# Performance work log

Hardware: AMD Instinct MI355X
Metric: run time of the kernel (lower is better)

Reference implementation:

```python
import jax, jax.numpy as jnp
import numpy as np

N_USERS = 100000
N_ITEMS = 50000
DIM = 64
N_EDGES = 1000000
N_NODES = N_USERS + N_ITEMS


def setup_inputs() -> dict:
    key = jax.random.key(0)
    k1, k2, k3 = jax.random.split(key, 3)
    # nn.init.normal_(std=0.1)
    user_emb = jax.random.normal(k1, (N_USERS, DIM), dtype=jnp.float32) * 0.1
    item_emb = jax.random.normal(k2, (N_ITEMS, DIM), dtype=jnp.float32) * 0.1
    edge_index = jax.random.randint(k3, (2, N_EDGES), 0, N_NODES, dtype=jnp.int32)
    return {"user_emb": user_emb, "item_emb": item_emb,
            "edge_index": edge_index, "n_layers": 3}


def reference(user_emb, item_emb, edge_index, n_layers):
    """LightGCN.computer(): n_layers of LGConv with uniform-alpha residual sum."""
    num_users = user_emb.shape[0]
    x = jnp.concatenate([user_emb, item_emb], axis=0)  # [N, d]
    n = x.shape[0]
    src, dst = edge_index[0], edge_index[1]

    # gcn_norm without self-loops (PyG LGConv default): deg from dst (in-degree)
    deg = jax.ops.segment_sum(jnp.ones_like(dst, dtype=x.dtype), dst,
                              num_segments=n)  # [N]
    dinv = jnp.where(deg > 0, jax.lax.rsqrt(jnp.maximum(deg, 1.0)), 0.0)
    norm = dinv[src] * dinv[dst]  # [E]

    alpha = 1.0 / (n_layers + 1)
    out = x * alpha
    for _ in range(n_layers):
        msg = x[src] * norm[:, None]                          # gather + scale [E, d]
        x = jax.ops.segment_sum(msg, dst, num_segments=n)     # scatter-add  [N, d]
        out = out + x * alpha
    users = out[:num_users]
    items = out[num_users:]
    return users, items
```

## Files before the change

kernel.cpp:

```cpp
#include <hip/hip_runtime.h>


#define N_USERS_C 100000
#define NNODES_C  150000
#define DIM_C     64
#define NLAYERS_C 3

#define BSHIFT    10
#define BSIZE     1024
#define NB_BUCKET ((NNODES_C + BSIZE - 1) >> BSHIFT)
#define EPB       4096
#define NBLK_E    ((1000000 + EPB - 1) / EPB)
#define HIST_N    (NB_BUCKET * NBLK_E)
#define SCAN_L1B  ((HIST_N + 1023) / 1024)


__device__ __forceinline__ float bf2f(unsigned short u) {
    union { unsigned int i; float f; } c;
    c.i = ((unsigned int)u) << 16;
    return c.f;
}

__device__ __forceinline__ unsigned short f2bf(float f) {
    union { float f; unsigned int i; } c;
    c.f = f;
    unsigned int x = c.i;
    return (unsigned short)((x + 0x7fffu + ((x >> 16) & 1u)) >> 16);
}


__global__ void k_hist(const int* __restrict__ dst, int* __restrict__ hist, int nE) {
    __shared__ int sh[NB_BUCKET];
    for (int i = threadIdx.x; i < NB_BUCKET; i += 256) sh[i] = 0;
    __syncthreads();
    int gEnd = min((int)(blockIdx.x + 1) * (EPB / 4), nE / 4);
    for (int g = blockIdx.x * (EPB / 4) + threadIdx.x; g < gEnd; g += 256) {
        int4 d4 = *(const int4*)(dst + g * 4);
        atomicAdd(&sh[d4.x >> BSHIFT], 1);
        atomicAdd(&sh[d4.y >> BSHIFT], 1);
        atomicAdd(&sh[d4.z >> BSHIFT], 1);
        atomicAdd(&sh[d4.w >> BSHIFT], 1);
    }
    __syncthreads();
    for (int b = threadIdx.x; b < NB_BUCKET; b += 256)
        hist[b * NBLK_E + blockIdx.x] = sh[b];
}

__global__ void k_scan_l1(int* __restrict__ hist, int* __restrict__ l1sum) {
    __shared__ int sd[1024];
    int t = threadIdx.x;
    int i = blockIdx.x * 1024 + t;
    int v = (i < HIST_N) ? hist[i] : 0;
    sd[t] = v;
    __syncthreads();
    for (int o = 1; o < 1024; o <<= 1) {
        int u = (t >= o) ? sd[t - o] : 0;
        __syncthreads();
        sd[t] += u;
        __syncthreads();
    }
    if (i < HIST_N) hist[i] = sd[t] - v;
    if (t == 1023) l1sum[blockIdx.x] = sd[1023];
}

__global__ void k_scan_l2add(int* __restrict__ hist, const int* __restrict__ l1sum) {
    __shared__ int s_pre;
    int t = threadIdx.x;
    if (t < 64) {
        int v = (t < (int)blockIdx.x && t < SCAN_L1B) ? l1sum[t] : 0;
        #pragma unroll
        for (int m = 1; m < 64; m <<= 1) v += __shfl_xor(v, m);
        if (t == 0) s_pre = v;
    }
    __syncthreads();
    int i = blockIdx.x * 1024 + t;
    if (i < HIST_N) hist[i] += s_pre;
}

__global__ void k_bucket(const int* __restrict__ src, const int* __restrict__ dst,
                         const int* __restrict__ histS, unsigned int* __restrict__ staged,
                         int nE) {
    __shared__ int sc[NB_BUCKET];
    for (int b = threadIdx.x; b < NB_BUCKET; b += 256)
        sc[b] = histS[b * NBLK_E + blockIdx.x];
    __syncthreads();
    int gEnd = min((int)(blockIdx.x + 1) * (EPB / 4), nE / 4);
    for (int g = blockIdx.x * (EPB / 4) + threadIdx.x; g < gEnd; g += 256) {
        int4 s4 = *(const int4*)(src + g * 4);
        int4 d4 = *(const int4*)(dst + g * 4);
        int p;
        p = atomicAdd(&sc[d4.x >> BSHIFT], 1);
        staged[p] = ((unsigned int)s4.x << BSHIFT) | (unsigned int)(d4.x & (BSIZE - 1));
        p = atomicAdd(&sc[d4.y >> BSHIFT], 1);
        staged[p] = ((unsigned int)s4.y << BSHIFT) | (unsigned int)(d4.y & (BSIZE - 1));
        p = atomicAdd(&sc[d4.z >> BSHIFT], 1);
        staged[p] = ((unsigned int)s4.z << BSHIFT) | (unsigned int)(d4.z & (BSIZE - 1));
        p = atomicAdd(&sc[d4.w >> BSHIFT], 1);
        staged[p] = ((unsigned int)s4.w << BSHIFT) | (unsigned int)(d4.w & (BSIZE - 1));
    }
}

__global__ void k_csr(const int* __restrict__ histS, const unsigned int* __restrict__ staged,
                      int* __restrict__ off, int* __restrict__ csrS,
                      const float* __restrict__ ue, const float* __restrict__ ie,
                      unsigned short* __restrict__ T0,
                      int nE, int nNodes) {
    __shared__ int s_deg[BSIZE];
    __shared__ int s_off[BSIZE];
    __shared__ int s_p[256];
    int b = blockIdx.x;
    int t = threadIdx.x;
    int base = histS[b * NBLK_E];
    int end  = (b + 1 < NB_BUCKET) ? histS[(b + 1) * NBLK_E] : nE;
    int cnt  = end - base;

    for (int i = t; i < BSIZE; i += 256) s_deg[i] = 0;
    __syncthreads();
    for (int k = t; k < cnt; k += 256) {
        unsigned int w = staged[base + k];
        atomicAdd(&s_deg[w & (BSIZE - 1)], 1);
    }
    __syncthreads();
    int l0 = s_deg[t * 4], l1 = s_deg[t * 4 + 1], l2 = s_deg[t * 4 + 2], l3 = s_deg[t * 4 + 3];
    int psum = l0 + l1 + l2 + l3;
    s_p[t] = psum;
    __syncthreads();
    for (int o = 1; o < 256; o <<= 1) {
        int v = (t >= o) ? s_p[t - o] : 0;
        __syncthreads();
        s_p[t] += v;
        __syncthreads();
    }
    int ex = s_p[t] - psum;
    s_off[t * 4]     = ex;
    s_off[t * 4 + 1] = ex + l0;
    s_off[t * 4 + 2] = ex + l0 + l1;
    s_off[t * 4 + 3] = ex + l0 + l1 + l2;
    __syncthreads();
    int nodeBase = b << BSHIFT;
    for (int i = t; i < BSIZE; i += 256) {
        int node = nodeBase + i;
        if (node < nNodes) off[node] = base + s_off[i];
    }
    if (b == 0 && t == 0) off[nNodes] = nE;

    for (int g = t; g < BSIZE * 8; g += 256) {
        int nl   = g >> 3;
        int node = nodeBase + nl;
        if (node < nNodes) {
            int dg = s_deg[nl];
            float dv = (dg > 0) ? rsqrtf((float)dg) : 0.0f;
            int sub = g & 7;
            const float* eb = (node < N_USERS_C)
                ? (ue + (size_t)node * DIM_C + sub * 8)
                : (ie + (size_t)(node - N_USERS_C) * DIM_C + sub * 8);
            float4 A = *(const float4*)(eb);
            float4 B = *(const float4*)(eb + 4);
            uint4 o;
            o.x = (unsigned int)f2bf(A.x * dv) | ((unsigned int)f2bf(A.y * dv) << 16);
            o.y = (unsigned int)f2bf(A.z * dv) | ((unsigned int)f2bf(A.w * dv) << 16);
            o.z = (unsigned int)f2bf(B.x * dv) | ((unsigned int)f2bf(B.y * dv) << 16);
            o.w = (unsigned int)f2bf(B.z * dv) | ((unsigned int)f2bf(B.w * dv) << 16);
            *(uint4*)(T0 + (size_t)node * DIM_C + sub * 8) = o;
        }
    }
    __syncthreads();
    for (int i = t; i < BSIZE; i += 256) s_deg[i] = s_off[i];
    __syncthreads();
    for (int k = t; k < cnt; k += 256) {
        unsigned int w = staged[base + k];
        int slot = base + atomicAdd(&s_deg[w & (BSIZE - 1)], 1);
        csrS[slot] = (int)(w >> BSHIFT);
    }
}


__device__ __forceinline__ void add8(float* a, uint4 v) {
    a[0] += bf2f((unsigned short)(v.x & 0xffff));
    a[1] += bf2f((unsigned short)(v.x >> 16));
    a[2] += bf2f((unsigned short)(v.y & 0xffff));
    a[3] += bf2f((unsigned short)(v.y >> 16));
    a[4] += bf2f((unsigned short)(v.z & 0xffff));
    a[5] += bf2f((unsigned short)(v.z >> 16));
    a[6] += bf2f((unsigned short)(v.w & 0xffff));
    a[7] += bf2f((unsigned short)(v.w >> 16));
}

__device__ __forceinline__ void fma8(float* a, uint4 v, float w) {
    a[0] += w * bf2f((unsigned short)(v.x & 0xffff));
    a[1] += w * bf2f((unsigned short)(v.x >> 16));
    a[2] += w * bf2f((unsigned short)(v.y & 0xffff));
    a[3] += w * bf2f((unsigned short)(v.y >> 16));
    a[4] += w * bf2f((unsigned short)(v.z & 0xffff));
    a[5] += w * bf2f((unsigned short)(v.z >> 16));
    a[6] += w * bf2f((unsigned short)(v.w & 0xffff));
    a[7] += w * bf2f((unsigned short)(v.w >> 16));
}

template <int FINAL>
__global__ void k_gather(const int* __restrict__ off, const int* __restrict__ csrS,
                         const unsigned short* __restrict__ T,
                         unsigned short* __restrict__ Tn,
                         const float* __restrict__ ue, const float* __restrict__ ie,
                         const unsigned short* __restrict__ T1,
                         const unsigned short* __restrict__ T2,
                         float* __restrict__ outp, float alpha, int nNodes) {
    int t = blockIdx.x * blockDim.x + threadIdx.x;
    int w = t >> 6;
    int lane = t & 63;
    int half = lane >> 5;
    int sub  = lane & 31;
    int slot = sub >> 3;
    int q    = sub & 7;
    int node = w * 2 + half;
    if (node >= nNodes) return;

    int b = off[node];
    int e = off[node + 1];

    float a[8] = {0.f, 0.f, 0.f, 0.f, 0.f, 0.f, 0.f, 0.f};

    for (int jj = b; jj < e; jj += 4) {
        int j = jj + slot;
        if (j < e) {
            int s = csrS[j];
            uint4 v = *(const uint4*)(T + (size_t)s * DIM_C + q * 8);
            add8(a, v);
        }
    }

    #pragma unroll
    for (int m = 8; m <= 16; m <<= 1) {
        #pragma unroll
        for (int k = 0; k < 8; ++k) a[k] += __shfl_xor(a[k], m);
    }

    if (slot == 0) {
        size_t idx = (size_t)node * DIM_C + q * 8;
        float degf = (float)(e - b);
        if (FINAL) {
            float sd = sqrtf(degf);
            float dv = (e > b) ? rsqrtf(degf) : 0.0f;
            const float* ob = (node < N_USERS_C)
                ? (ue + (size_t)node * DIM_C + q * 8)
                : (ie + (size_t)(node - N_USERS_C) * DIM_C + q * 8);
            float4 x0a = *(const float4*)(ob);
            float4 x0b = *(const float4*)(ob + 4);
            uint4 u1 = *(const uint4*)(T1 + idx);
            uint4 u2 = *(const uint4*)(T2 + idx);
            float r[8] = {0.f, 0.f, 0.f, 0.f, 0.f, 0.f, 0.f, 0.f};
            fma8(r, u1, sd);
            fma8(r, u2, sd);
            float4 o0, o1;
            o0.x = alpha * (x0a.x + r[0] + dv * a[0]);
            o0.y = alpha * (x0a.y + r[1] + dv * a[1]);
            o0.z = alpha * (x0a.z + r[2] + dv * a[2]);
            o0.w = alpha * (x0a.w + r[3] + dv * a[3]);
            o1.x = alpha * (x0b.x + r[4] + dv * a[4]);
            o1.y = alpha * (x0b.y + r[5] + dv * a[5]);
            o1.z = alpha * (x0b.z + r[6] + dv * a[6]);
            o1.w = alpha * (x0b.w + r[7] + dv * a[7]);
            *(float4*)(outp + idx)     = o0;
            *(float4*)(outp + idx + 4) = o1;
        } else {
            float inv = (e > b) ? (1.0f / degf) : 0.0f;
            uint4 o;
            o.x = (unsigned int)f2bf(a[0] * inv) | ((unsigned int)f2bf(a[1] * inv) << 16);
            o.y = (unsigned int)f2bf(a[2] * inv) | ((unsigned int)f2bf(a[3] * inv) << 16);
            o.z = (unsigned int)f2bf(a[4] * inv) | ((unsigned int)f2bf(a[5] * inv) << 16);
            o.w = (unsigned int)f2bf(a[6] * inv) | ((unsigned int)f2bf(a[7] * inv) << 16);
            *(uint4*)(Tn + idx) = o;
        }
    }
}


__global__ void k_count_deg_fb(const int* __restrict__ dst, int* __restrict__ deg, int nE) {
    int e = blockIdx.x * blockDim.x + threadIdx.x;
    if (e < nE) atomicAdd(&deg[dst[e]], 1);
}

__global__ void k_dinv_fb(const int* __restrict__ deg, float* __restrict__ dinv, int n) {
    int i = blockIdx.x * blockDim.x + threadIdx.x;
    if (i < n) {
        int d = deg[i];
        dinv[i] = (d > 0) ? rsqrtf((float)d) : 0.0f;
    }
}

__global__ void k_init_fb(const float4* __restrict__ ue, const float4* __restrict__ ie,
                          float4* __restrict__ x, float4* __restrict__ out,
                          float alpha, int n4u, int n4) {
    int i = blockIdx.x * blockDim.x + threadIdx.x;
    if (i < n4) {
        float4 v = (i < n4u) ? ue[i] : ie[i - n4u];
        x[i] = v;
        out[i] = make_float4(v.x * alpha, v.y * alpha, v.z * alpha, v.w * alpha);
    }
}

__global__ void k_scatter(const int* __restrict__ src, const int* __restrict__ dst,
                          const float* __restrict__ dinv, const float* __restrict__ x,
                          float* __restrict__ y, int nE) {
    int t = blockIdx.x * blockDim.x + threadIdx.x;
    int e = t >> 4;
    int q = t & 15;
    if (e >= nE) return;
    int s = src[e];
    int d = dst[e];
    float w = dinv[s] * dinv[d];
    float4 v = *(const float4*)(x + (size_t)s * DIM_C + q * 4);
    float* yp = y + (size_t)d * DIM_C + q * 4;
    atomicAdd(yp + 0, v.x * w);
    atomicAdd(yp + 1, v.y * w);
    atomicAdd(yp + 2, v.z * w);
    atomicAdd(yp + 3, v.w * w);
}

__global__ void k_accum(const float4* __restrict__ y, float4* __restrict__ out,
                        float alpha, int n4) {
    int i = blockIdx.x * blockDim.x + threadIdx.x;
    if (i < n4) {
        float4 v = y[i];
        float4 o = out[i];
        o.x += v.x * alpha;
        o.y += v.y * alpha;
        o.z += v.z * alpha;
        o.w += v.w * alpha;
        out[i] = o;
    }
}


extern "C" void kernel_launch(void* const* d_in, const int* in_sizes, int n_in,
                              void* d_out, int out_size, void* d_ws, size_t ws_size,
                              hipStream_t stream) {
    const float* user_emb = (const float*)d_in[0];
    const float* item_emb = (const float*)d_in[1];
    const int*   edge     = (const int*)d_in[2];

    const int nE = in_sizes[2] / 2;
    const int* src = edge;
    const int* dst = edge + nE;

    const int nNodes = NNODES_C;
    const int nElems = nNodes * DIM_C;
    const int n4     = nElems / 4;
    const int n4u    = N_USERS_C * DIM_C / 4;
    const float alpha = 1.0f / (NLAYERS_C + 1);
    float* out = (float*)d_out;

    const size_t REQ = 66344448;

    char* ws = (char*)d_ws;

    if (ws_size >= REQ) {
        int*            hist   = (int*)           (ws);
        int*            l1sum  = (int*)           (ws + 144064);
        unsigned int*   staged = (unsigned int*)  (ws + 144320);
        int*            off    = (int*)           (ws + 4144320);
        int*            csrS   = (int*)           (ws + 4744336);
        unsigned short* T0     = (unsigned short*)(ws + 8744448);
        unsigned short* T1     = (unsigned short*)(ws + 27944448);
        unsigned short* T2     = (unsigned short*)(ws + 47144448);

        k_hist<<<NBLK_E, 256, 0, stream>>>(dst, hist, nE);
        k_scan_l1<<<SCAN_L1B, 1024, 0, stream>>>(hist, l1sum);
        k_scan_l2add<<<SCAN_L1B, 1024, 0, stream>>>(hist, l1sum);
        k_bucket<<<NBLK_E, 256, 0, stream>>>(src, dst, hist, staged, nE);
        k_csr<<<NB_BUCKET, 256, 0, stream>>>(hist, staged, off, csrS,
                                             user_emb, item_emb, T0, nE, nNodes);

        const int gwaves  = (nNodes + 1) / 2;
        const int gblocks = (gwaves * 64 + 255) / 256;
        k_gather<0><<<gblocks, 256, 0, stream>>>(off, csrS, T0, T1,
                                                 nullptr, nullptr, nullptr, nullptr,
                                                 nullptr, alpha, nNodes);
        k_gather<0><<<gblocks, 256, 0, stream>>>(off, csrS, T1, T2,
                                                 nullptr, nullptr, nullptr, nullptr,
                                                 nullptr, alpha, nNodes);
        k_gather<1><<<gblocks, 256, 0, stream>>>(off, csrS, T2, nullptr,
                                                 user_emb, item_emb, T1, T2,
                                                 out, alpha, nNodes);
    } else {
        int*   deg  = (int*)  (ws);
        float* dinv = (float*)(ws + 600000);
        float* xbuf = (float*)(ws + 1200000);
        float* ybuf = (float*)(ws + 1200000 + (size_t)nElems * 4);

        hipMemsetAsync(deg, 0, (size_t)nNodes * sizeof(int), stream);
        k_count_deg_fb<<<(nE + 255) / 256, 256, 0, stream>>>(dst, deg, nE);
        k_dinv_fb<<<(nNodes + 255) / 256, 256, 0, stream>>>(deg, dinv, nNodes);
        k_init_fb<<<(n4 + 255) / 256, 256, 0, stream>>>(
            (const float4*)user_emb, (const float4*)item_emb,
            (float4*)xbuf, (float4*)out, alpha, n4u, n4);

        float* xb = xbuf;
        float* yb = ybuf;
        const int scatterThreads = nE * 16;
        for (int l = 0; l < NLAYERS_C; ++l) {
            hipMemsetAsync(yb, 0, (size_t)nElems * sizeof(float), stream);
            k_scatter<<<(scatterThreads + 255) / 256, 256, 0, stream>>>(
                src, dst, dinv, xb, yb, nE);
            k_accum<<<(n4 + 255) / 256, 256, 0, stream>>>(
                (const float4*)yb, (float4*)out, alpha, n4);
            float* tmp = xb; xb = yb; yb = tmp;
        }
    }
}
```

Before: 162.9 us.

## Split embedding bf16 conversion out of CSR kernel and widen CSR blocks

The CSR build kernel now runs 1024 threads per bucket with a single-element-per-thread Hillis-Steele scan, and no longer performs the degree-scaled bf16 conversion of embeddings. That conversion moves into a separate fully parallel elementwise kernel that derives degree from the CSR offsets. The intent is to stop the roughly 147 CSR blocks from being bottlenecked on the 38 MB embedding read, and to spread that read across many more blocks. In exchange it adds a kernel launch and a 1024-step-wide scan that needs more barriers.

```diff
diff --git a/kernel.cpp b/kernel.cpp
--- a/kernel.cpp
+++ b/kernel.cpp
@@ -102,76 +102,62 @@
 
 __global__ void k_csr(const int* __restrict__ histS, const unsigned int* __restrict__ staged,
                       int* __restrict__ off, int* __restrict__ csrS,
-                      const float* __restrict__ ue, const float* __restrict__ ie,
-                      unsigned short* __restrict__ T0,
                       int nE, int nNodes) {
     __shared__ int s_deg[BSIZE];
-    __shared__ int s_off[BSIZE];
-    __shared__ int s_p[256];
+    __shared__ int s_scan[BSIZE];
     int b = blockIdx.x;
     int t = threadIdx.x;
     int base = histS[b * NBLK_E];
     int end  = (b + 1 < NB_BUCKET) ? histS[(b + 1) * NBLK_E] : nE;
     int cnt  = end - base;
 
-    for (int i = t; i < BSIZE; i += 256) s_deg[i] = 0;
-    __syncthreads();
-    for (int k = t; k < cnt; k += 256) {
+    s_deg[t] = 0;
+    __syncthreads();
+    for (int k = t; k < cnt; k += BSIZE) {
         unsigned int w = staged[base + k];
         atomicAdd(&s_deg[w & (BSIZE - 1)], 1);
     }
     __syncthreads();
-    int l0 = s_deg[t * 4], l1 = s_deg[t * 4 + 1], l2 = s_deg[t * 4 + 2], l3 = s_deg[t * 4 + 3];
-    int psum = l0 + l1 + l2 + l3;
-    s_p[t] = psum;
-    __syncthreads();
-    for (int o = 1; o < 256; o <<= 1) {
-        int v = (t >= o) ? s_p[t - o] : 0;
+    int v = s_deg[t];
+    s_scan[t] = v;
+    __syncthreads();
+    for (int o = 1; o < BSIZE; o <<= 1) {
+        int u = (t >= o) ? s_scan[t - o] : 0;
         __syncthreads();
-        s_p[t] += v;
+        s_scan[t] += u;
         __syncthreads();
     }
-    int ex = s_p[t] - psum;
-    s_off[t * 4]     = ex;
-    s_off[t * 4 + 1] = ex + l0;
-    s_off[t * 4 + 2] = ex + l0 + l1;
-    s_off[t * 4 + 3] = ex + l0 + l1 + l2;
-    __syncthreads();
-    int nodeBase = b << BSHIFT;
-    for (int i = t; i < BSIZE; i += 256) {
-        int node = nodeBase + i;
-        if (node < nNodes) off[node] = base + s_off[i];
-    }
+    int ex = s_scan[t] - v;
+    int node = (b << BSHIFT) + t;
+    if (node < nNodes) off[node] = base + ex;
     if (b == 0 && t == 0) off[nNodes] = nE;
-
-    for (int g = t; g < BSIZE * 8; g += 256) {
-        int nl   = g >> 3;
-        int node = nodeBase + nl;
-        if (node < nNodes) {
-            int dg = s_deg[nl];
-            float dv = (dg > 0) ? rsqrtf((float)dg) : 0.0f;
-            int sub = g & 7;
-            const float* eb = (node < N_USERS_C)
-                ? (ue + (size_t)node * DIM_C + sub * 8)
-                : (ie + (size_t)(node - N_USERS_C) * DIM_C + sub * 8);
-            float4 A = *(const float4*)(eb);
-            float4 B = *(const float4*)(eb + 4);
-            uint4 o;
-            o.x = (unsigned int)f2bf(A.x * dv) | ((unsigned int)f2bf(A.y * dv) << 16);
-            o.y = (unsigned int)f2bf(A.z * dv) | ((unsigned int)f2bf(A.w * dv) << 16);
-            o.z = (unsigned int)f2bf(B.x * dv) | ((unsigned int)f2bf(B.y * dv) << 16);
-            o.w = (unsigned int)f2bf(B.z * dv) | ((unsigned int)f2bf(B.w * dv) << 16);
-            *(uint4*)(T0 + (size_t)node * DIM_C + sub * 8) = o;
-        }
-    }
-    __syncthreads();
-    for (int i = t; i < BSIZE; i += 256) s_deg[i] = s_off[i];
-    __syncthreads();
-    for (int k = t; k < cnt; k += 256) {
+    s_deg[t] = ex;
+    __syncthreads();
+    for (int k = t; k < cnt; k += BSIZE) {
         unsigned int w = staged[base + k];
         int slot = base + atomicAdd(&s_deg[w & (BSIZE - 1)], 1);
         csrS[slot] = (int)(w >> BSHIFT);
     }
+}
+
+
+__global__ void k_cvt(const float4* __restrict__ ue, const float4* __restrict__ ie,
+                      const int* __restrict__ off, uint4* __restrict__ t0,
+                      int n8u, int n8) {
+    int i = blockIdx.x * blockDim.x + threadIdx.x;
+    if (i >= n8) return;
+    int node = i >> 3;
+    int dg = off[node + 1] - off[node];
+    float dv = (dg > 0) ? rsqrtf((float)dg) : 0.0f;
+    float4 a, b;
+    if (i < n8u) { a = ue[2 * i];         b = ue[2 * i + 1]; }
+    else         { a = ie[2 * (i - n8u)]; b = ie[2 * (i - n8u) + 1]; }
+    uint4 o;
+    o.x = (unsigned int)f2bf(a.x * dv) | ((unsigned int)f2bf(a.y * dv) << 16);
+    o.y = (unsigned int)f2bf(a.z * dv) | ((unsigned int)f2bf(a.w * dv) << 16);
+    o.z = (unsigned int)f2bf(b.x * dv) | ((unsigned int)f2bf(b.y * dv) << 16);
+    o.w = (unsigned int)f2bf(b.z * dv) | ((unsigned int)f2bf(b.w * dv) << 16);
+    t0[i] = o;
 }
 
 
@@ -368,8 +354,12 @@
         k_scan_l1<<<SCAN_L1B, 1024, 0, stream>>>(hist, l1sum);
         k_scan_l2add<<<SCAN_L1B, 1024, 0, stream>>>(hist, l1sum);
         k_bucket<<<NBLK_E, 256, 0, stream>>>(src, dst, hist, staged, nE);
-        k_csr<<<NB_BUCKET, 256, 0, stream>>>(hist, staged, off, csrS,
-                                             user_emb, item_emb, T0, nE, nNodes);
+        k_csr<<<NB_BUCKET, BSIZE, 0, stream>>>(hist, staged, off, csrS, nE, nNodes);
+
+        const int n8  = nElems / 8;
+        const int n8u = N_USERS_C * DIM_C / 8;
+        k_cvt<<<(n8 + 255) / 256, 256, 0, stream>>>(
+            (const float4*)user_emb, (const float4*)item_emb, off, (uint4*)T0, n8u, n8);
 
         const int gwaves  = (nNodes + 1) / 2;
         const int gblocks = (gwaves * 64 + 255) / 256;
```

Result: faster. 148.1 us (-9.1%).
